# Performance work log

Measured on AMD Instinct MI355X. Metric: run time of the kernel, lower is better.

## Reference

```python
import jax, jax.numpy as jnp
import numpy as np

B, C, H, W = 4, 64, 64, 64
C2 = 2 * C
CR = C2 // 16  # SE bottleneck

def setup_inputs() -> dict:
    key = jax.random.key(0)
    ks = jax.random.split(key, 8)
    stdv = 1.0 / np.sqrt(C)
    return {
        "x1": jax.random.normal(ks[0], (B, C, H, W), jnp.float32),
        "x2": jax.random.normal(ks[1], (B, C, H, W), jnp.float32),
        "weight": jax.random.uniform(ks[2], (C, C), jnp.float32, -stdv, stdv),
        "weight2": jax.random.uniform(ks[3], (C, C), jnp.float32, -stdv, stdv),
        "ca_fc1": jax.random.normal(ks[4], (CR, C2), jnp.float32) * 0.05,  # 1x1 conv as matrix
        "ca_fc2": jax.random.normal(ks[5], (C2, CR), jnp.float32) * 0.05,
        "conv_w": jax.random.normal(ks[6], (C, C2), jnp.float32) * 0.05,  # 1x1 conv 2C->C
        "conv_b": jnp.zeros((C,), jnp.float32),
    }

def reference(x1, x2, weight, weight2, ca_fc1, ca_fc2, conv_w, conv_b):
    b, c, h, w = x2.shape
    n = h * w
    a1 = x1.reshape(b, c, n)  # x1 flattened [B,C,N]
    a2 = x2.reshape(b, c, n)  # x2 flattened [B,C,N]
    # Non-local branch: f = theta_x @ phi_x = a1^T @ a2 -> [B,N,N]
    f = jnp.einsum('bcn,bcm->bnm', a1, a2)
    adj = jax.nn.softmax(f, axis=-1)
    support = jnp.einsum('bcn,cd->bnd', a2, weight)  # g_x @ W, [B,N,C]
    y = jnp.einsum('bnm,bmd->bnd', adj, support)     # adj @ support
    y = y.transpose(0, 2, 1).reshape(b, c, h, w)
    # Channel-affinity branch: c_x = a_x @ b_x -> [B,C,C]
    c_x = jnp.einsum('bcn,bdn->bcd', a1, a2)
    support2 = jnp.einsum('bcd,de->bce', c_x, weight2)   # [B,C,C]
    y2 = jnp.einsum('bcd,bdn->bcn', support2, a1).reshape(b, c, h, w)
    z = jnp.concatenate([y, y2], axis=1)  # [B,2C,H,W]
    # ChannelAttention: global max pool -> fc1 -> relu -> fc2 -> sigmoid
    mp = jnp.max(z, axis=(2, 3))                       # [B,2C]
    hdn = jax.nn.relu(jnp.einsum('be,re->br', mp, ca_fc1))
    v = jax.nn.sigmoid(jnp.einsum('br,er->be', hdn, ca_fc2))  # [B,2C]
    out = z * v[:, :, None, None] + z
    out = jnp.einsum('behw,oe->bohw', out, conv_w) + conv_b[None, :, None, None]
    return out
```

## Files before the change

kernel.cpp:

```cpp
#include <hip/hip_runtime.h>
#include <hip/hip_bf16.h>
#include <math.h>

#define B_   4
#define C_   64
#define N_   4096
#define C2_  128

using frag  = __attribute__((ext_vector_type(8))) short;
using f32x4 = __attribute__((ext_vector_type(4))) float;
using f4    = __attribute__((ext_vector_type(4))) float;

__device__ __forceinline__ unsigned short f2bf(float f) {
  unsigned int u = __float_as_uint(f);
  u += 0x7fffu + ((u >> 16) & 1u);
  return (unsigned short)(u >> 16);
}
__device__ __forceinline__ float bf2f(unsigned short h) {
  return __uint_as_float(((unsigned int)h) << 16);
}
__device__ __forceinline__ unsigned int pkbf(float a, float b) {
  __hip_bfloat16 ha = __float2bfloat16(a), hb = __float2bfloat16(b);
  unsigned short ua, ub;
  __builtin_memcpy(&ua, &ha, 2);
  __builtin_memcpy(&ub, &hb, 2);
  return (unsigned int)ua | ((unsigned int)ub << 16);
}
__device__ __forceinline__ frag pk8(f4 lo, f4 hi) {
  frag f;
  unsigned int* u = (unsigned int*)&f;
  u[0] = pkbf(lo.x, lo.y);
  u[1] = pkbf(lo.z, lo.w);
  u[2] = pkbf(hi.x, hi.y);
  u[3] = pkbf(hi.z, hi.w);
  return f;
}
__device__ __forceinline__ f4 max4(f4 a, f4 b) {
  return (f4){fmaxf(a.x, b.x), fmaxf(a.y, b.y), fmaxf(a.z, b.z), fmaxf(a.w, b.w)};
}

__global__ __launch_bounds__(256) void prep_kernel(const float* __restrict__ x1,
                                                   const float* __restrict__ x2,
                                                   unsigned short* __restrict__ a1t,
                                                   unsigned short* __restrict__ a2t,
                                                   float* __restrict__ cxp) {
  __shared__ float tA[64 * 65];
  __shared__ float tB[64 * 65];
  int b = blockIdx.y, n0 = blockIdx.x * 64, tid = threadIdx.x;
  int wave = tid >> 6, lane = tid & 63, l16 = lane & 15, lq = lane >> 4;
  {
    int n = tid & 63, cq = tid >> 6;
#pragma unroll
    for (int k = 0; k < 16; ++k) {
      int c = cq + 4 * k;
      tA[c * 65 + n] = x2[((size_t)(b * C_ + c)) * N_ + n0 + n];
      tB[c * 65 + n] = x1[((size_t)(b * C_ + c)) * N_ + n0 + n];
    }
  }
  __syncthreads();
  {
    int c = tid & 63, nq = tid >> 6;
#pragma unroll
    for (int k = 0; k < 16; ++k) {
      int n2 = nq + 4 * k;
      a2t[((size_t)b * N_ + n0 + n2) * C_ + c] = f2bf(tA[c * 65 + n2]);
      a1t[((size_t)b * N_ + n0 + n2) * C_ + c] = f2bf(tB[c * 65 + n2]);
    }
  }
  {
    int dd = 16 * wave + l16;
    frag afr[2];
#pragma unroll
    for (int ks = 0; ks < 2; ++ks) {
      float w0[8];
#pragma unroll
      for (int j = 0; j < 8; ++j) w0[j] = tA[dd * 65 + ks * 32 + lq * 8 + j];
      afr[ks] = pk8((f4){w0[0], w0[1], w0[2], w0[3]}, (f4){w0[4], w0[5], w0[6], w0[7]});
    }
    f32x4 acc[4];
#pragma unroll
    for (int cg = 0; cg < 4; ++cg) acc[cg] = (f32x4){0.f, 0.f, 0.f, 0.f};
#pragma unroll
    for (int cg = 0; cg < 4; ++cg) {
      int cc = cg * 16 + l16;
#pragma unroll
      for (int ks = 0; ks < 2; ++ks) {
        float w0[8];
#pragma unroll
        for (int j = 0; j < 8; ++j) w0[j] = tB[cc * 65 + ks * 32 + lq * 8 + j];
        frag bfr = pk8((f4){w0[0], w0[1], w0[2], w0[3]}, (f4){w0[4], w0[5], w0[6], w0[7]});
        acc[cg] = __builtin_amdgcn_mfma_f32_16x16x32_bf16(afr[ks], bfr, acc[cg], 0, 0, 0);
      }
    }
    float* op = cxp + ((size_t)(b * 64 + blockIdx.x)) * 4096;
#pragma unroll
    for (int cg = 0; cg < 4; ++cg)
#pragma unroll
      for (int r = 0; r < 4; ++r)
        op[(16 * wave + 4 * lq + r) * 64 + cg * 16 + l16] = acc[cg][r];
  }
}

__global__ __launch_bounds__(256) void support_mm_kernel(const float* __restrict__ weight,
                                                         const unsigned short* __restrict__ a2t,
                                                         unsigned short* __restrict__ vT) {
  __shared__ float Wl[64 * 65];
  int b = blockIdx.y, n0 = blockIdx.x * 32, tid = threadIdx.x;
  int wave = tid >> 6, lane = tid & 63, l16 = lane & 15, lq = lane >> 4;
#pragma unroll
  for (int k = 0; k < 16; ++k) {
    int lin = tid + 256 * k;
    Wl[(lin >> 6) * 65 + (lin & 63)] = weight[lin];
  }
  frag b0[2], b1[2];
#pragma unroll
  for (int ng = 0; ng < 2; ++ng) {
    const unsigned short* bp = a2t + ((size_t)b * N_ + n0 + ng * 16 + l16) * C_;
    b0[ng] = *(const frag*)(bp + lq * 8);
    b1[ng] = *(const frag*)(bp + 32 + lq * 8);
  }
  __syncthreads();
  int dd = 16 * wave + l16;
  frag aw[2];
#pragma unroll
  for (int ks = 0; ks < 2; ++ks) {
    float wv[8];
#pragma unroll
    for (int j = 0; j < 8; ++j) wv[j] = Wl[(ks * 32 + lq * 8 + j) * 65 + dd];
    aw[ks] = pk8((f4){wv[0], wv[1], wv[2], wv[3]}, (f4){wv[4], wv[5], wv[6], wv[7]});
  }
  f32x4 acc[2];
#pragma unroll
  for (int ng = 0; ng < 2; ++ng) {
    acc[ng] = (f32x4){0.f, 0.f, 0.f, 0.f};
    acc[ng] = __builtin_amdgcn_mfma_f32_16x16x32_bf16(aw[0], b0[ng], acc[ng], 0, 0, 0);
    acc[ng] = __builtin_amdgcn_mfma_f32_16x16x32_bf16(aw[1], b1[ng], acc[ng], 0, 0, 0);
  }
#pragma unroll
  for (int ng = 0; ng < 2; ++ng)
#pragma unroll
    for (int r = 0; r < 4; ++r)
      vT[((size_t)(b * C_) + 16 * wave + 4 * lq + r) * N_ + n0 + ng * 16 + l16] =
          f2bf(acc[ng][r]);
}

__global__ __launch_bounds__(256) void cxred_kernel(const float* __restrict__ cxp,
                                                    float* __restrict__ cx) {
  int idx = blockIdx.x * 256 + threadIdx.x;
  int b = idx >> 12, r = idx & 4095;
  const float* p = cxp + (size_t)b * 64 * 4096 + r;
  float s = 0.f;
#pragma unroll 8
  for (int sg = 0; sg < 64; ++sg) s += p[(size_t)sg * 4096];
  cx[idx] = s;
}

__global__ __launch_bounds__(256) void s2bf_kernel(const float* __restrict__ cx,
                                                   const float* __restrict__ w2,
                                                   unsigned short* __restrict__ s2bf) {
  __shared__ float cxl[4096];
  __shared__ float w2l[4096];
  int b = blockIdx.x, tid = threadIdx.x;
#pragma unroll
  for (int k = 0; k < 16; ++k) {
    int lin = tid + 256 * k;
    cxl[lin] = cx[(size_t)b * 4096 + lin];
    w2l[lin] = w2[lin];
  }
  __syncthreads();
  int c = tid & 63, eg = tid >> 6;
  float acc[16];
#pragma unroll
  for (int i = 0; i < 16; ++i) acc[i] = 0.f;
  for (int d = 0; d < 64; ++d) {
    float a = cxl[d * 64 + c];
#pragma unroll
    for (int i = 0; i < 16; ++i) acc[i] += a * w2l[d * 64 + eg * 16 + i];
  }
  unsigned short* op = s2bf + (size_t)b * 4096 + c * 64 + eg * 16;
#pragma unroll
  for (int i = 0; i < 8; ++i)
    *(unsigned int*)(op + 2 * i) = pkbf(acc[2 * i], acc[2 * i + 1]);
}

template <int SEG>
__global__ __launch_bounds__(512) void attn_kernel(const unsigned short* __restrict__ a1t,
                                                   const unsigned short* __restrict__ a2t,
                                                   const unsigned short* __restrict__ vT,
                                                   float* __restrict__ z,
                                                   unsigned short* __restrict__ Opart,
                                                   float* __restrict__ ml) {
  __shared__ unsigned short Kt[2][64 * 64];
  __shared__ unsigned short Vt[2][64 * 64];
  __shared__ uint2 Pl[8][16 * 16];

  const int b = blockIdx.y, n0 = blockIdx.x * 128, tid = threadIdx.x;
  const int seg = (SEG > 1) ? blockIdx.z : 0;
  const int wave = tid >> 6, lane = tid & 63;
  const int l16 = lane & 15, lq = lane >> 4;
  const int NT = N_ / SEG / 64;
  const int mbase = seg * (N_ / SEG);

  const unsigned short* qbase = a1t + ((size_t)b * N_ + n0 + wave * 16 + l16) * C_;
  frag qa0 = *(const frag*)(qbase + lq * 8);
  frag qa1 = *(const frag*)(qbase + 32 + lq * 8);

  f32x4 O[4];
#pragma unroll
  for (int i = 0; i < 4; ++i) O[i] = (f32x4){0.f, 0.f, 0.f, 0.f};
  float m_l = -1e30f, l_l = 0.f;

  const unsigned short* a2b = a2t + (size_t)b * N_ * C_;
  const unsigned short* vTb = vT + (size_t)b * C_ * N_;
  char* Pw = (char*)&Pl[wave][0];
  const int swzP = (l16 & 7) << 4;

  const int srow = tid >> 3, scb = tid & 7;
  const int kswz = (scb * 16) ^ ((srow & 7) << 4);

  frag k0 = *(const frag*)(a2b + (size_t)(mbase + srow) * C_ + scb * 8);
  frag v0 = *(const frag*)(vTb + (size_t)srow * N_ + mbase + scb * 8);
  *(frag*)((char*)&Kt[0][0] + srow * 128 + kswz) = k0;
  *(frag*)((char*)&Vt[0][0] + srow * 128 + kswz) = v0;
  __syncthreads();

  int cur = 0;
  for (int t = 0; t < NT; ++t, cur ^= 1) {
    if (t + 1 < NT) {
      int mn = mbase + (t + 1) * 64;
      k0 = *(const frag*)(a2b + (size_t)(mn + srow) * C_ + scb * 8);
      v0 = *(const frag*)(vTb + (size_t)srow * N_ + mn + scb * 8);
    }

    f32x4 S[4];
    __builtin_amdgcn_s_setprio(1);
#pragma unroll
    for (int ms = 0; ms < 4; ++ms) {
      int m = ms * 16 + l16;
      int swz = (m & 7) << 4;
      frag kb0 = *(const frag*)((char*)&Kt[cur][0] + m * 128 + ((lq * 16) ^ swz));
      frag kb1 = *(const frag*)((char*)&Kt[cur][0] + m * 128 + ((64 + lq * 16) ^ swz));
      f32x4 acc = (f32x4){0.f, 0.f, 0.f, 0.f};
      acc = __builtin_amdgcn_mfma_f32_16x16x32_bf16(kb0, qa0, acc, 0, 0, 0);
      acc = __builtin_amdgcn_mfma_f32_16x16x32_bf16(kb1, qa1, acc, 0, 0, 0);
      S[ms] = acc;
    }
    __builtin_amdgcn_s_setprio(0);

    float mx0 = fmaxf(fmaxf(S[0][0], S[0][1]), fmaxf(S[0][2], S[0][3]));
    float mx1 = fmaxf(fmaxf(S[1][0], S[1][1]), fmaxf(S[1][2], S[1][3]));
    float mx2 = fmaxf(fmaxf(S[2][0], S[2][1]), fmaxf(S[2][2], S[2][3]));
    float mx3 = fmaxf(fmaxf(S[3][0], S[3][1]), fmaxf(S[3][2], S[3][3]));
    float mx = fmaxf(fmaxf(mx0, mx1), fmaxf(mx2, mx3));
    mx = fmaxf(mx, __shfl_xor(mx, 16, 64));
    mx = fmaxf(mx, __shfl_xor(mx, 32, 64));

    if (!__all(mx <= m_l + 8.f)) {
      float mn = fmaxf(m_l, mx);
      float sc = __expf(m_l - mn);
      m_l = mn;
      l_l *= sc;
      float scb_[4];
#pragma unroll
      for (int r = 0; r < 4; ++r) scb_[r] = __shfl(sc, 20 * lq + r, 64);
#pragma unroll
      for (int ds = 0; ds < 4; ++ds)
#pragma unroll
        for (int r = 0; r < 4; ++r) O[ds][r] *= scb_[r];
    }

    float p[16];
    float rs = 0.f;
#pragma unroll
    for (int ms = 0; ms < 4; ++ms)
#pragma unroll
      for (int r = 0; r < 4; ++r) {
        float e = __expf(S[ms][r] - m_l);
        p[ms * 4 + r] = e;
        rs += e;
      }
    rs += __shfl_xor(rs, 16, 64);
    rs += __shfl_xor(rs, 32, 64);
    l_l += rs;

#pragma unroll
    for (int ms = 0; ms < 4; ++ms) {
      uint2 w;
      w.x = pkbf(p[ms * 4 + 0], p[ms * 4 + 1]);
      w.y = pkbf(p[ms * 4 + 2], p[ms * 4 + 3]);
      *(uint2*)(Pw + l16 * 128 + ((32 * ms + 8 * lq) ^ swzP)) = w;
    }
    asm volatile("s_waitcnt lgkmcnt(0)" ::: "memory");
    __builtin_amdgcn_sched_barrier(0);

    frag pa0 = *(const frag*)(Pw + l16 * 128 + ((lq * 16) ^ swzP));
    frag pa1 = *(const frag*)(Pw + l16 * 128 + ((64 + lq * 16) ^ swzP));
    __builtin_amdgcn_s_setprio(1);
#pragma unroll
    for (int ds = 0; ds < 4; ++ds) {
      int d = ds * 16 + l16;
      int swz = (d & 7) << 4;
      frag vb0 = *(const frag*)((char*)&Vt[cur][0] + d * 128 + ((lq * 16) ^ swz));
      frag vb1 = *(const frag*)((char*)&Vt[cur][0] + d * 128 + ((64 + lq * 16) ^ swz));
      O[ds] = __builtin_amdgcn_mfma_f32_16x16x32_bf16(pa0, vb0, O[ds], 0, 0, 0);
      O[ds] = __builtin_amdgcn_mfma_f32_16x16x32_bf16(pa1, vb1, O[ds], 0, 0, 0);
    }
    __builtin_amdgcn_s_setprio(0);

    if (t + 1 < NT) {
      *(frag*)((char*)&Kt[cur ^ 1][0] + srow * 128 + kswz) = k0;
      *(frag*)((char*)&Vt[cur ^ 1][0] + srow * 128 + kswz) = v0;
      __syncthreads();
    }
  }

  if (SEG > 1) {
    size_t base = (size_t)(b * SEG + seg) * N_ + n0 + wave * 16;
    if (lq == 0) {
      ml[(base + l16) * 2]     = m_l;
      ml[(base + l16) * 2 + 1] = l_l;
    }
#pragma unroll
    for (int r = 0; r < 4; ++r)
#pragma unroll
      for (int ds = 0; ds < 4; ++ds)
        Opart[(base + lq * 4 + r) * 64 + ds * 16 + l16] = f2bf(O[ds][r]);
  } else {
    float inv[4];
#pragma unroll
    for (int r = 0; r < 4; ++r) inv[r] = 1.f / __shfl(l_l, 20 * lq + r, 64);
#pragma unroll
    for (int ds = 0; ds < 4; ++ds)
#pragma unroll
      for (int r = 0; r < 4; ++r)
        z[((size_t)b * N_ + n0 + wave * 16 + lq * 4 + r) * 128 + ds * 16 + l16] = O[ds][r] * inv[r];
  }
}

template <int SEG>
__global__ __launch_bounds__(256) void combine_kernel(const unsigned short* __restrict__ Opart,
                                                      const float* __restrict__ ml,
                                                      float* __restrict__ z,
                                                      float* __restrict__ mppA) {
  __shared__ float zsm[64][65];
  int b = blockIdx.y, tid = threadIdx.x;
  int nr = tid >> 2;
  int n = blockIdx.x * 64 + nr;
  int dq = (tid & 3) * 16;
  float mv[SEG], lv[SEG], M = -1e30f;
#pragma unroll
  for (int s = 0; s < SEG; ++s) {
    size_t r = (size_t)(b * SEG + s) * N_ + n;
    mv[s] = ml[r * 2];
    lv[s] = ml[r * 2 + 1];
    M = fmaxf(M, mv[s]);
  }
  float acc[16];
#pragma unroll
  for (int j = 0; j < 16; ++j) acc[j] = 0.f;
  float l = 0.f;
#pragma unroll
  for (int s = 0; s < SEG; ++s) {
    float w = __expf(mv[s] - M);
    l += w * lv[s];
    const unsigned short* op = Opart + ((size_t)(b * SEG + s) * N_ + n) * 64 + dq;
    frag p0 = *(const frag*)(op);
    frag p1 = *(const frag*)(op + 8);
#pragma unroll
    for (int j = 0; j < 8; ++j) {
      acc[j]     += w * bf2f((unsigned short)p0[j]);
      acc[8 + j] += w * bf2f((unsigned short)p1[j]);
    }
  }
  float inv = 1.f / l;
  float* zp = z + ((size_t)b * N_ + n) * 128 + dq;
#pragma unroll
  for (int k = 0; k < 4; ++k) {
    f4 res = (f4){acc[4 * k] * inv, acc[4 * k + 1] * inv,
                  acc[4 * k + 2] * inv, acc[4 * k + 3] * inv};
    *(f4*)(zp + k * 4) = res;
    zsm[nr][dq + 4 * k]     = res.x;
    zsm[nr][dq + 4 * k + 1] = res.y;
    zsm[nr][dq + 4 * k + 2] = res.z;
    zsm[nr][dq + 4 * k + 3] = res.w;
  }
  __syncthreads();
  if (tid < 64) {
    float mx = -1e30f;
    for (int nn = 0; nn < 64; ++nn) mx = fmaxf(mx, zsm[nn][tid]);
    mppA[((size_t)b * 64 + blockIdx.x) * 64 + tid] = mx;
  }
}

__global__ __launch_bounds__(256) void mpA_kernel(const float* __restrict__ z,
                                                  float* __restrict__ mppA) {
  __shared__ float red[4][64];
  int b = blockIdx.y, n0 = blockIdx.x * 64, tid = threadIdx.x;
  int e = tid & 63, g = tid >> 6;
  float mx = -1e30f;
#pragma unroll
  for (int k = 0; k < 16; ++k)
    mx = fmaxf(mx, z[((size_t)b * N_ + n0 + g + 4 * k) * 128 + e]);
  red[g][e] = mx;
  __syncthreads();
  if (tid < 64)
    mppA[((size_t)b * 64 + blockIdx.x) * 64 + tid] =
        fmaxf(fmaxf(red[0][tid], red[1][tid]), fmaxf(red[2][tid], red[3][tid]));
}

__global__ __launch_bounds__(256) void y2_kernel(const unsigned short* __restrict__ s2bf,
                                                 const unsigned short* __restrict__ a1t,
                                                 float* __restrict__ z,
                                                 float* __restrict__ mppB) {
  __shared__ f4 red[4][4][16];
  int b = blockIdx.y, n0 = blockIdx.x * 32, tid = threadIdx.x;
  int wave = tid >> 6, lane = tid & 63, l16 = lane & 15, lq = lane >> 4;
  const unsigned short* s2r = s2bf + (size_t)b * 4096 + (16 * wave + l16) * 64;
  frag sa0 = *(const frag*)(s2r + lq * 8);
  frag sa1 = *(const frag*)(s2r + 32 + lq * 8);
  f4 mx = (f4){-1e30f, -1e30f, -1e30f, -1e30f};
#pragma unroll
  for (int j = 0; j < 2; ++j) {
    const unsigned short* bp = a1t + ((size_t)b * N_ + n0 + 16 * j + l16) * 64;
    frag b0 = *(const frag*)(bp + lq * 8);
    frag b1 = *(const frag*)(bp + 32 + lq * 8);
    f32x4 acc = (f32x4){0.f, 0.f, 0.f, 0.f};
    acc = __builtin_amdgcn_mfma_f32_16x16x32_bf16(sa0, b0, acc, 0, 0, 0);
    acc = __builtin_amdgcn_mfma_f32_16x16x32_bf16(sa1, b1, acc, 0, 0, 0);
    *(f4*)(z + ((size_t)b * N_ + n0 + 16 * j + l16) * 128 + 64 + 16 * wave + 4 * lq) = acc;
#pragma unroll
    for (int r = 0; r < 4; ++r) mx[r] = fmaxf(mx[r], acc[r]);
  }
  red[wave][lq][l16] = mx;
  __syncthreads();
  if (tid < 64) {
    int w = tid >> 4, q = (tid >> 2) & 3, r = tid & 3;
    float m = -1e30f;
#pragma unroll
    for (int l = 0; l < 16; ++l) m = fmaxf(m, red[w][q][l][r]);
    mppB[((size_t)b * 128 + blockIdx.x) * 64 + 16 * w + 4 * q + r] = m;
  }
}

__global__ __launch_bounds__(256) void ca2_kernel(const float* __restrict__ mppA,
                                                  const float* __restrict__ mppB,
                                                  const float* __restrict__ fc1,
                                                  const float* __restrict__ fc2,
                                                  float* __restrict__ vbuf) {
  __shared__ f4 red4[256];
  __shared__ float mpl[128];
  __shared__ float red2[8][33];
  __shared__ float hl[8];
  int b = blockIdx.x, t = threadIdx.x;
  {
    const f4* src = (const f4*)(mppA + (size_t)b * 64 * 64);
    f4 m = src[t];
    m = max4(m, src[t + 256]);
    m = max4(m, src[t + 512]);
    m = max4(m, src[t + 768]);
    red4[t] = m;
  }
  __syncthreads();
  if (t < 16) {
    f4 m = red4[t];
#pragma unroll
    for (int j = 1; j < 16; ++j) m = max4(m, red4[t + 16 * j]);
    *(f4*)&mpl[t * 4] = m;
  }
  __syncthreads();
  {
    const f4* src = (const f4*)(mppB + (size_t)b * 128 * 64);
    f4 m = src[t];
#pragma unroll
    for (int k = 1; k < 8; ++k) m = max4(m, src[t + 256 * k]);
    red4[t] = m;
  }
  __syncthreads();
  if (t < 16) {
    f4 m = red4[t];
#pragma unroll
    for (int j = 1; j < 16; ++j) m = max4(m, red4[t + 16 * j]);
    *(f4*)&mpl[64 + t * 4] = m;
  }
  __syncthreads();
  {
    int r = t >> 5, j = t & 31;
    const f4 mv = *(const f4*)&mpl[j * 4];
    const f4 wv = *(const f4*)(fc1 + r * 128 + j * 4);
    red2[r][j] = mv.x * wv.x + mv.y * wv.y + mv.z * wv.z + mv.w * wv.w;
  }
  __syncthreads();
  if (t < 8) {
    float s = 0.f;
#pragma unroll
    for (int j = 0; j < 32; ++j) s += red2[t][j];
    hl[t] = fmaxf(s, 0.f);
  }
  __syncthreads();
  if (t < 128) {
    float s = 0.f;
    const float* f2r = fc2 + t * 8;
#pragma unroll
    for (int r = 0; r < 8; ++r) s += hl[r] * f2r[r];
    vbuf[b * 128 + t] = 1.f + 1.f / (1.f + __expf(-s));
  }
}

__global__ __launch_bounds__(256) void conv_kernel(const float* __restrict__ z,
                                                   const float* __restrict__ vbuf,
                                                   const float* __restrict__ conv_w,
                                                   const float* __restrict__ conv_b,
                                                   float* __restrict__ out) {
  __shared__ unsigned short zv[32 * 128];
  int b = blockIdx.y, n0 = blockIdx.x * 32, tid = threadIdx.x;
  int wave = tid >> 6, lane = tid & 63, l16 = lane & 15, lq = lane >> 4;
  {
    int e4 = tid & 31;
    f4 vq = *(const f4*)(vbuf + b * 128 + e4 * 4);
#pragma unroll
    for (int k = 0; k < 4; ++k) {
      int row = (tid >> 5) + 8 * k;
      f4 zq = *(const f4*)(z + ((size_t)(b * N_) + n0 + row) * 128 + e4 * 4);
      zq *= vq;
      uint2 w;
      w.x = pkbf(zq.x, zq.y);
      w.y = pkbf(zq.z, zq.w);
      *(uint2*)((char*)zv + row * 256 + ((e4 * 8) ^ ((row & 7) << 4))) = w;
    }
  }
  const float* cwr = conv_w + (size_t)(16 * wave + l16) * 128 + lq * 8;
  frag aw[4];
#pragma unroll
  for (int ks = 0; ks < 4; ++ks)
    aw[ks] = pk8(*(const f4*)(cwr + ks * 32), *(const f4*)(cwr + ks * 32 + 4));
  __syncthreads();
  f32x4 acc[2];
#pragma unroll
  for (int ng = 0; ng < 2; ++ng) acc[ng] = (f32x4){0.f, 0.f, 0.f, 0.f};
#pragma unroll
  for (int ng = 0; ng < 2; ++ng) {
    int n = ng * 16 + l16;
    int swz = (n & 7) << 4;
#pragma unroll
    for (int ks = 0; ks < 4; ++ks) {
      frag bz = *(const frag*)((char*)zv + n * 256 + ((ks * 64 + lq * 16) ^ swz));
      acc[ng] = __builtin_amdgcn_mfma_f32_16x16x32_bf16(aw[ks], bz, acc[ng], 0, 0, 0);
    }
  }
#pragma unroll
  for (int r = 0; r < 4; ++r) {
    int o = 16 * wave + 4 * lq + r;
    float bias = conv_b[o];
#pragma unroll
    for (int ng = 0; ng < 2; ++ng)
      out[((size_t)(b * C_ + o)) * N_ + n0 + ng * 16 + l16] = acc[ng][r] + bias;
  }
}

extern "C" void kernel_launch(void* const* d_in, const int* in_sizes, int n_in,
                              void* d_out, int out_size, void* d_ws, size_t ws_size,
                              hipStream_t stream) {
  const float* x1      = (const float*)d_in[0];
  const float* x2      = (const float*)d_in[1];
  const float* weight  = (const float*)d_in[2];
  const float* weight2 = (const float*)d_in[3];
  const float* fc1     = (const float*)d_in[4];
  const float* fc2     = (const float*)d_in[5];
  const float* conv_w  = (const float*)d_in[6];
  const float* conv_b  = (const float*)d_in[7];
  float* out = (float*)d_out;

  char* ws = (char*)d_ws;
  unsigned short* a1t = (unsigned short*)(ws + 0);
  unsigned short* a2t = (unsigned short*)(ws + 2097152);
  float* mppA = (float*)(ws + 2097152);
  float* mppB = (float*)(ws + 2162688);
  unsigned short* s2bf = (unsigned short*)(ws + 2293760);
  unsigned short* vT  = (unsigned short*)(ws + 4194304);
  float* z    = (float*)(ws + 6291456);
  float* cxp  = (float*)(ws + 6291456);
  float* cx   = (float*)(ws + 14680064);
  float* vbuf = (float*)(ws + 14745600);
  unsigned short* Opart = (unsigned short*)(ws + 14764544);
  float* ml4  = (float*)(ws + 23153152);
  float* ml8  = (float*)(ws + 31541760);
  const bool seg8 = ws_size >= 32590336ull;
  const bool seg4 = ws_size >= 23677440ull;

  prep_kernel<<<dim3(64, 4), 256, 0, stream>>>(x1, x2, a1t, a2t, cxp);
  support_mm_kernel<<<dim3(128, 4), 256, 0, stream>>>(weight, a2t, vT);
  cxred_kernel<<<dim3(64), 256, 0, stream>>>(cxp, cx);
  if (seg8) {
    attn_kernel<8><<<dim3(32, 4, 8), 512, 0, stream>>>(a1t, a2t, vT, z, Opart, ml8);
    combine_kernel<8><<<dim3(64, 4), 256, 0, stream>>>(Opart, ml8, z, mppA);
  } else if (seg4) {
    attn_kernel<4><<<dim3(32, 4, 4), 512, 0, stream>>>(a1t, a2t, vT, z, Opart, ml4);
    combine_kernel<4><<<dim3(64, 4), 256, 0, stream>>>(Opart, ml4, z, mppA);
  } else {
    attn_kernel<1><<<dim3(32, 4), 512, 0, stream>>>(a1t, a2t, vT, z, nullptr, nullptr);
    mpA_kernel<<<dim3(64, 4), 256, 0, stream>>>(z, mppA);
  }
  s2bf_kernel<<<dim3(4), 256, 0, stream>>>(cx, weight2, s2bf);
  y2_kernel<<<dim3(128, 4), 256, 0, stream>>>(s2bf, a1t, z, mppB);
  ca2_kernel<<<dim3(4), 256, 0, stream>>>(mppA, mppB, fc1, fc2, vbuf);
  conv_kernel<<<dim3(128, 4), 256, 0, stream>>>(z, vbuf, conv_w, conv_b, out);
}
```

Baseline: 75.76 us.

## Fuse support matmul into prep kernel and drop 8-segment attention split

Computes the support product (weight applied to x2) inside prep_kernel from the x2 tile already held in shared memory, which removes a separate launch and the re-read of a2t from global memory. Separately, removes the 8-segment split-K attention path so that the 4-segment path is the largest used. This reduces attention parallelism when the workspace is large and adds a 16KB shared buffer to prep_kernel, which may lower its occupancy.

```diff
diff --git a/kernel.cpp b/kernel.cpp
--- a/kernel.cpp
+++ b/kernel.cpp
@@ -41,11 +41,14 @@
 
 __global__ __launch_bounds__(256) void prep_kernel(const float* __restrict__ x1,
                                                    const float* __restrict__ x2,
+                                                   const float* __restrict__ weight,
                                                    unsigned short* __restrict__ a1t,
                                                    unsigned short* __restrict__ a2t,
+                                                   unsigned short* __restrict__ vT,
                                                    float* __restrict__ cxp) {
   __shared__ float tA[64 * 65];
   __shared__ float tB[64 * 65];
+  __shared__ float Wl[64 * 65];
   int b = blockIdx.y, n0 = blockIdx.x * 64, tid = threadIdx.x;
   int wave = tid >> 6, lane = tid & 63, l16 = lane & 15, lq = lane >> 4;
   {
@@ -55,6 +58,7 @@
       int c = cq + 4 * k;
       tA[c * 65 + n] = x2[((size_t)(b * C_ + c)) * N_ + n0 + n];
       tB[c * 65 + n] = x1[((size_t)(b * C_ + c)) * N_ + n0 + n];
+      Wl[c * 65 + n] = weight[c * 64 + n];
     }
   }
   __syncthreads();
@@ -99,49 +103,33 @@
       for (int r = 0; r < 4; ++r)
         op[(16 * wave + 4 * lq + r) * 64 + cg * 16 + l16] = acc[cg][r];
   }
-}
-
-__global__ __launch_bounds__(256) void support_mm_kernel(const float* __restrict__ weight,
-                                                         const unsigned short* __restrict__ a2t,
-                                                         unsigned short* __restrict__ vT) {
-  __shared__ float Wl[64 * 65];
-  int b = blockIdx.y, n0 = blockIdx.x * 32, tid = threadIdx.x;
-  int wave = tid >> 6, lane = tid & 63, l16 = lane & 15, lq = lane >> 4;
-#pragma unroll
-  for (int k = 0; k < 16; ++k) {
-    int lin = tid + 256 * k;
-    Wl[(lin >> 6) * 65 + (lin & 63)] = weight[lin];
-  }
-  frag b0[2], b1[2];
-#pragma unroll
-  for (int ng = 0; ng < 2; ++ng) {
-    const unsigned short* bp = a2t + ((size_t)b * N_ + n0 + ng * 16 + l16) * C_;
-    b0[ng] = *(const frag*)(bp + lq * 8);
-    b1[ng] = *(const frag*)(bp + 32 + lq * 8);
-  }
-  __syncthreads();
-  int dd = 16 * wave + l16;
-  frag aw[2];
-#pragma unroll
-  for (int ks = 0; ks < 2; ++ks) {
-    float wv[8];
-#pragma unroll
-    for (int j = 0; j < 8; ++j) wv[j] = Wl[(ks * 32 + lq * 8 + j) * 65 + dd];
-    aw[ks] = pk8((f4){wv[0], wv[1], wv[2], wv[3]}, (f4){wv[4], wv[5], wv[6], wv[7]});
-  }
-  f32x4 acc[2];
-#pragma unroll
-  for (int ng = 0; ng < 2; ++ng) {
-    acc[ng] = (f32x4){0.f, 0.f, 0.f, 0.f};
-    acc[ng] = __builtin_amdgcn_mfma_f32_16x16x32_bf16(aw[0], b0[ng], acc[ng], 0, 0, 0);
-    acc[ng] = __builtin_amdgcn_mfma_f32_16x16x32_bf16(aw[1], b1[ng], acc[ng], 0, 0, 0);
-  }
-#pragma unroll
-  for (int ng = 0; ng < 2; ++ng)
-#pragma unroll
-    for (int r = 0; r < 4; ++r)
-      vT[((size_t)(b * C_) + 16 * wave + 4 * lq + r) * N_ + n0 + ng * 16 + l16] =
-          f2bf(acc[ng][r]);
+  {
+    int dd = 16 * wave + l16;
+    frag aw[2];
+#pragma unroll
+    for (int ks = 0; ks < 2; ++ks) {
+      float wv[8];
+#pragma unroll
+      for (int j = 0; j < 8; ++j) wv[j] = Wl[(ks * 32 + lq * 8 + j) * 65 + dd];
+      aw[ks] = pk8((f4){wv[0], wv[1], wv[2], wv[3]}, (f4){wv[4], wv[5], wv[6], wv[7]});
+    }
+#pragma unroll
+    for (int ng = 0; ng < 4; ++ng) {
+      int nn = ng * 16 + l16;
+      f32x4 acc = (f32x4){0.f, 0.f, 0.f, 0.f};
+#pragma unroll
+      for (int ks = 0; ks < 2; ++ks) {
+        float bx[8];
+#pragma unroll
+        for (int j = 0; j < 8; ++j) bx[j] = tA[(ks * 32 + lq * 8 + j) * 65 + nn];
+        frag bf = pk8((f4){bx[0], bx[1], bx[2], bx[3]}, (f4){bx[4], bx[5], bx[6], bx[7]});
+        acc = __builtin_amdgcn_mfma_f32_16x16x32_bf16(aw[ks], bf, acc, 0, 0, 0);
+      }
+#pragma unroll
+      for (int r = 0; r < 4; ++r)
+        vT[((size_t)(b * C_) + 16 * wave + 4 * lq + r) * N_ + n0 + nn] = f2bf(acc[r]);
+    }
+  }
 }
 
 __global__ __launch_bounds__(256) void cxred_kernel(const float* __restrict__ cxp,
@@ -582,20 +570,14 @@
   float* cx   = (float*)(ws + 14680064);
   float* vbuf = (float*)(ws + 14745600);
   unsigned short* Opart = (unsigned short*)(ws + 14764544);
-  float* ml4  = (float*)(ws + 23153152);
-  float* ml8  = (float*)(ws + 31541760);
-  const bool seg8 = ws_size >= 32590336ull;
+  float* ml   = (float*)(ws + 23153152);
   const bool seg4 = ws_size >= 23677440ull;
 
-  prep_kernel<<<dim3(64, 4), 256, 0, stream>>>(x1, x2, a1t, a2t, cxp);
-  support_mm_kernel<<<dim3(128, 4), 256, 0, stream>>>(weight, a2t, vT);
+  prep_kernel<<<dim3(64, 4), 256, 0, stream>>>(x1, x2, weight, a1t, a2t, vT, cxp);
   cxred_kernel<<<dim3(64), 256, 0, stream>>>(cxp, cx);
-  if (seg8) {
-    attn_kernel<8><<<dim3(32, 4, 8), 512, 0, stream>>>(a1t, a2t, vT, z, Opart, ml8);
-    combine_kernel<8><<<dim3(64, 4), 256, 0, stream>>>(Opart, ml8, z, mppA);
-  } else if (seg4) {
-    attn_kernel<4><<<dim3(32, 4, 4), 512, 0, stream>>>(a1t, a2t, vT, z, Opart, ml4);
-    combine_kernel<4><<<dim3(64, 4), 256, 0, stream>>>(Opart, ml4, z, mppA);
+  if (seg4) {
+    attn_kernel<4><<<dim3(32, 4, 4), 512, 0, stream>>>(a1t, a2t, vT, z, Opart, ml);
+    combine_kernel<4><<<dim3(64, 4), 256, 0, stream>>>(Opart, ml, z, mppA);
   } else {
     attn_kernel<1><<<dim3(32, 4), 512, 0, stream>>>(a1t, a2t, vT, z, nullptr, nullptr);
     mpA_kernel<<<dim3(64, 4), 256, 0, stream>>>(z, mppA);
```

After: 71.36 us. 5.8% less time.
